# Kernel optimization log

Hardware: AMD Instinct MI355X
Metric: run time of the kernel (lower is better)

The kernel has to match this reference:

```python
import jax, jax.numpy as jnp
import numpy as np

N_NODES = 50000
N_EDGES = 800000
N_GRAPHS = 64
IN_DIM = 128
HID = 32
HEADS = 4
EDGE_DIM = 8
OUT = 10


def setup_inputs() -> dict:
    key = jax.random.key(0)
    ks = jax.random.split(key, 20)
    s = 0.1
    inp = {
        "x": jax.random.normal(ks[0], (N_NODES, IN_DIM), jnp.float32),
        "edge_index": jax.random.randint(ks[1], (2, N_EDGES), 0, N_NODES, jnp.int32),
        "edge_attr": jax.random.normal(ks[2], (N_EDGES, EDGE_DIM), jnp.float32),
        "batch": jnp.sort(jax.random.randint(ks[3], (N_NODES,), 0, N_GRAPHS, jnp.int32)),
        # conv1: heads=4, out=32
        "W1": jax.random.normal(ks[4], (IN_DIM, HEADS * HID), jnp.float32) * s,
        "att_src1": jax.random.normal(ks[5], (HEADS, HID), jnp.float32) * s,
        "att_dst1": jax.random.normal(ks[6], (HEADS, HID), jnp.float32) * s,
        "We1": jax.random.normal(ks[7], (EDGE_DIM, HEADS * HID), jnp.float32) * s,
        "att_e1": jax.random.normal(ks[8], (HEADS, HID), jnp.float32) * s,
        "b1": jnp.zeros((HEADS * HID,), jnp.float32),
        # conv2: heads=1, out=32
        "W2": jax.random.normal(ks[9], (HEADS * HID, HID), jnp.float32) * s,
        "att_src2": jax.random.normal(ks[10], (1, HID), jnp.float32) * s,
        "att_dst2": jax.random.normal(ks[11], (1, HID), jnp.float32) * s,
        "We2": jax.random.normal(ks[12], (EDGE_DIM, HID), jnp.float32) * s,
        "att_e2": jax.random.normal(ks[13], (1, HID), jnp.float32) * s,
        "b2": jnp.zeros((HID,), jnp.float32),
        # MLP head
        "W3": jax.random.normal(ks[14], (HID, HID // 2), jnp.float32) * s,
        "b3": jnp.zeros((HID // 2,), jnp.float32),
        "W4": jax.random.normal(ks[15], (HID // 2, OUT), jnp.float32) * s,
        "b4": jnp.zeros((OUT,), jnp.float32),
    }
    return inp


def _gat_conv(x, src, dst, eattr, W, a_s, a_d, We, a_e, b, H, C, N):
    """PyG GATConv math (self-loops already appended to src/dst/eattr)."""
    h = (x @ W).reshape(-1, H, C)            # [N,H,C]
    e = (eattr @ We).reshape(-1, H, C)       # [E,H,C]
    al_s = jnp.sum(h * a_s, -1)              # [N,H]
    al_d = jnp.sum(h * a_d, -1)              # [N,H]
    alpha = al_s[src] + al_d[dst] + jnp.sum(e * a_e, -1)   # [E,H]
    alpha = jax.nn.leaky_relu(alpha, 0.2)
    # segment softmax over incoming edges of each dst node
    m = jax.ops.segment_max(alpha, dst, num_segments=N)
    ealpha = jnp.exp(alpha - m[dst])
    denom = jax.ops.segment_sum(ealpha, dst, num_segments=N)
    ealpha = ealpha / (denom[dst] + 1e-16)
    msg = h[src] * ealpha[:, :, None]        # [E,H,C]
    out = jax.ops.segment_sum(msg, dst, num_segments=N)  # [N,H,C]
    return out.reshape(N, H * C) + b


def _forward(x, edge_index, edge_attr, batch,
             W1, att_src1, att_dst1, We1, att_e1, b1,
             W2, att_src2, att_dst2, We2, att_e2, b2,
             W3, b3, W4, b4):
    N = x.shape[0]
    src, dst = edge_index[0], edge_index[1]
    # add_self_loops with fill_value='mean': loop attr = mean of incoming edge_attr
    cnt = jax.ops.segment_sum(jnp.ones((src.shape[0],), x.dtype), dst, num_segments=N)
    loop_attr = jax.ops.segment_sum(edge_attr, dst, num_segments=N) / jnp.maximum(cnt, 1.0)[:, None]
    ar = jnp.arange(N, dtype=src.dtype)
    src2 = jnp.concatenate([src, ar])
    dst2 = jnp.concatenate([dst, ar])
    eattr2 = jnp.concatenate([edge_attr, loop_attr], axis=0)

    h = _gat_conv(x, src2, dst2, eattr2, W1, att_src1, att_dst1, We1, att_e1, b1, HEADS, HID, N)
    h = jax.nn.elu(h)
    h = _gat_conv(h, src2, dst2, eattr2, W2, att_src2, att_dst2, We2, att_e2, b2, 1, HID, N)
    h = jax.nn.elu(h)
    # global mean pool per graph
    gsum = jax.ops.segment_sum(h, batch, num_segments=N_GRAPHS)
    gcnt = jax.ops.segment_sum(jnp.ones((N,), h.dtype), batch, num_segments=N_GRAPHS)
    g = gsum / jnp.maximum(gcnt, 1.0)[:, None]
    # MLP head (eval mode: dropout is identity)
    z = jax.nn.relu(g @ W3 + b3)
    return z @ W4 + b4


def reference(x, edge_index, edge_attr, batch,
              W1, att_src1, att_dst1, We1, att_e1, b1,
              W2, att_src2, att_dst2, We2, att_e2, b2,
              W3, b3, W4, b4):
    return _forward(x, edge_index, edge_attr, batch,
                    W1, att_src1, att_dst1, We1, att_e1, b1,
                    W2, att_src2, att_dst2, We2, att_e2, b2,
                    W3, b3, W4, b4)
```

## Files before the change

### kernel.cpp

```cpp
#include <hip/hip_runtime.h>
#include <hip/hip_bf16.h>
#include <math.h>

#define N_NODES 50000
#define N_EDGES 800000
#define N_GRAPHS 64
#define IN_DIM 128
#define HID 32
#define HEADS 4
#define EDGE_DIM 8
#define OUT_DIM 10
#define HC 128
#define NB 196
#define G1H 782

__device__ __forceinline__ float leaky(float x){ return x >= 0.f ? x : 0.2f*x; }
__device__ __forceinline__ float elu_f(float x){ return x > 0.f ? x : __expf(x)-1.f; }

__device__ __forceinline__ float bf2f(unsigned short u){
  union { unsigned int i; float f; } v; v.i = ((unsigned int)u) << 16; return v.f;
}
__device__ __forceinline__ unsigned short f2bf(float f){
  union { float f; unsigned int i; } v; v.f = f;
  unsigned int r = v.i + 0x7FFF + ((v.i >> 16) & 1);
  return (unsigned short)(r >> 16);
}

__device__ __forceinline__ void gemm1_body(int bb, float* xs, float* ws,
    const float* __restrict__ x, const float* __restrict__ W1,
    const float* __restrict__ as1, const float* __restrict__ ad1,
    unsigned short* __restrict__ h1b, float* __restrict__ als1, float* __restrict__ ald1){
  int t = threadIdx.x;
  int cg = t & 15, c8 = cg*8, qb = (t >> 4)*2;
  int base = bb * 32;
  for (int i = t; i < 1024; i += 256){
    int node = base + (i >> 5);
    int col = (i & 31) * 4;
    float4 v = make_float4(0,0,0,0);
    if (node < N_NODES) v = *(const float4*)&x[node*IN_DIM + col];
    *(float4*)&xs[(i>>5)*128 + col] = v;
  }
  float acc[2][8];
  #pragma unroll
  for (int q = 0; q < 2; q++)
    #pragma unroll
    for (int i = 0; i < 8; i++) acc[q][i] = 0.f;

  for (int kb = 0; kb < 128; kb += 32){
    __syncthreads();
    for (int i = t; i < 1024; i += 256)
      *(float4*)&ws[i*4] = *(const float4*)&W1[kb*128 + i*4];
    __syncthreads();
    #pragma unroll 8
    for (int k = 0; k < 32; k++){
      float4 w0 = *(float4*)&ws[k*128 + c8];
      float4 w1 = *(float4*)&ws[k*128 + c8 + 4];
      #pragma unroll
      for (int q = 0; q < 2; q++){
        float xv = xs[(qb + q)*128 + kb + k];
        acc[q][0] = fmaf(xv, w0.x, acc[q][0]);
        acc[q][1] = fmaf(xv, w0.y, acc[q][1]);
        acc[q][2] = fmaf(xv, w0.z, acc[q][2]);
        acc[q][3] = fmaf(xv, w0.w, acc[q][3]);
        acc[q][4] = fmaf(xv, w1.x, acc[q][4]);
        acc[q][5] = fmaf(xv, w1.y, acc[q][5]);
        acc[q][6] = fmaf(xv, w1.z, acc[q][6]);
        acc[q][7] = fmaf(xv, w1.w, acc[q][7]);
      }
    }
  }
  int head = cg >> 2;
  float asv[8], adv[8];
  #pragma unroll
  for (int i = 0; i < 8; i++){ asv[i] = as1[c8 + i]; adv[i] = ad1[c8 + i]; }
  #pragma unroll
  for (int q = 0; q < 2; q++){
    int n = base + qb + q;
    if (n >= N_NODES) continue;
    float sa = 0.f, sd = 0.f;
    #pragma unroll
    for (int i = 0; i < 8; i++){
      sa = fmaf(acc[q][i], asv[i], sa);
      sd = fmaf(acc[q][i], adv[i], sd);
    }
    sa += __shfl_xor(sa, 1); sd += __shfl_xor(sd, 1);
    sa += __shfl_xor(sa, 2); sd += __shfl_xor(sd, 2);
    uint4 pk;
    pk.x = (unsigned int)f2bf(acc[q][0]) | ((unsigned int)f2bf(acc[q][1]) << 16);
    pk.y = (unsigned int)f2bf(acc[q][2]) | ((unsigned int)f2bf(acc[q][3]) << 16);
    pk.z = (unsigned int)f2bf(acc[q][4]) | ((unsigned int)f2bf(acc[q][5]) << 16);
    pk.w = (unsigned int)f2bf(acc[q][6]) | ((unsigned int)f2bf(acc[q][7]) << 16);
    *(uint4*)&h1b[n*HC + c8] = pk;
    if ((cg & 3) == 0){ als1[n*4 + head] = sa; ald1[n*4 + head] = sd; }
  }
}

__global__ __launch_bounds__(256) void k_f1(const int* __restrict__ dst, int* __restrict__ cnt,
    int* __restrict__ rank,
    const float* __restrict__ x, const float* __restrict__ W1,
    const float* __restrict__ as1, const float* __restrict__ ad1,
    unsigned short* __restrict__ h1b, float* __restrict__ als1, float* __restrict__ ald1){
  __shared__ float smem[8192];
  int m = blockIdx.x % 5, r = blockIdx.x / 5;
  if (m < 4){
    int e = (r*4 + m)*256 + threadIdx.x;
    if (e < N_EDGES) rank[e] = atomicAdd(&cnt[dst[e]], 1);
    return;
  }
  gemm1_body(r, smem, smem + 4096, x, W1, as1, ad1, h1b, als1, ald1);
}

__global__ __launch_bounds__(256) void k_blocksum(const int* __restrict__ cnt, int* __restrict__ bsum){
  __shared__ int sh[256];
  int n = blockIdx.x*256 + threadIdx.x;
  sh[threadIdx.x] = (n < N_NODES) ? cnt[n] : 0;
  __syncthreads();
  for (int off = 128; off > 0; off >>= 1){
    if (threadIdx.x < off) sh[threadIdx.x] += sh[threadIdx.x + off];
    __syncthreads();
  }
  if (threadIdx.x == 0) bsum[blockIdx.x] = sh[0];
}

__global__ __launch_bounds__(256) void k_scanb(const int* __restrict__ bsum, int* __restrict__ bpre){
  __shared__ int sh[256];
  int t = threadIdx.x;
  int v = (t < NB) ? bsum[t] : 0;
  sh[t] = v; __syncthreads();
  for (int off = 1; off < 256; off <<= 1){
    int u = (t >= off) ? sh[t-off] : 0;
    __syncthreads();
    sh[t] += u;
    __syncthreads();
  }
  if (t < NB) bpre[t] = sh[t] - v;
}

__global__ __launch_bounds__(256) void k_rowptr(const int* __restrict__ cnt, const int* __restrict__ bpre,
    int* __restrict__ rowptr){
  __shared__ int sh[256];
  int t = threadIdx.x; int n = blockIdx.x*256 + t;
  int c = (n < N_NODES) ? cnt[n] : 0;
  sh[t] = c; __syncthreads();
  for (int off = 1; off < 256; off <<= 1){
    int u = (t >= off) ? sh[t-off] : 0;
    __syncthreads();
    sh[t] += u;
    __syncthreads();
  }
  int incl = sh[t];
  if (n < N_NODES){
    rowptr[n] = bpre[blockIdx.x] + incl - c;
  }
  if (n == N_NODES-1) rowptr[N_NODES] = bpre[blockIdx.x] + incl;
}

__global__ __launch_bounds__(256) void k_f2(const int* __restrict__ src, const int* __restrict__ dst,
    const int* __restrict__ rank, const int* __restrict__ rowptr,
    const float* __restrict__ eattr,
    const float* __restrict__ We1, const float* __restrict__ ae1w,
    const float* __restrict__ We2, const float* __restrict__ ae2w,
    int4* __restrict__ rec,
    const float* __restrict__ x, const float* __restrict__ W1,
    const float* __restrict__ as1, const float* __restrict__ ad1,
    unsigned short* __restrict__ h1b, float* __restrict__ als1, float* __restrict__ ald1){
  __shared__ float smem[8192];
  int m = blockIdx.x % 5, r = blockIdx.x / 5;
  if (m < 4){
    int t = threadIdx.x;
    if (t < 32){
      int d = t >> 2, h = t & 3;
      float s = 0.f;
      for (int c = 0; c < 32; c++) s = fmaf(We1[d*128 + h*32 + c], ae1w[h*32 + c], s);
      smem[d*4 + h] = s;
    } else if (t < 40){
      int d = t - 32;
      float s = 0.f;
      for (int c = 0; c < 32; c++) s = fmaf(We2[d*32 + c], ae2w[c], s);
      smem[32 + d] = s;
    }
    __syncthreads();
    int e = (r*4 + m)*256 + t;
    if (e >= N_EDGES) return;
    int sv = src[e], d = dst[e], rk = rank[e];
    float4 x0 = *(const float4*)&eattr[e*8];
    float4 x1 = *(const float4*)&eattr[e*8+4];
    int pos = rowptr[d] + rk;
    float ea[8] = {x0.x,x0.y,x0.z,x0.w,x1.x,x1.y,x1.z,x1.w};
    float4 rr = make_float4(0,0,0,0);
    float r2 = 0.f;
    #pragma unroll
    for (int dd = 0; dd < 8; dd++){
      rr.x = fmaf(ea[dd], smem[dd*4+0], rr.x);
      rr.y = fmaf(ea[dd], smem[dd*4+1], rr.y);
      rr.z = fmaf(ea[dd], smem[dd*4+2], rr.z);
      rr.w = fmaf(ea[dd], smem[dd*4+3], rr.w);
      r2   = fmaf(ea[dd], smem[32+dd], r2);
    }
    int4 rv;
    rv.x = sv;
    rv.y = (int)((unsigned int)f2bf(rr.x) | ((unsigned int)f2bf(rr.y) << 16));
    rv.z = (int)((unsigned int)f2bf(rr.z) | ((unsigned int)f2bf(rr.w) << 16));
    rv.w = __float_as_int(r2);
    rec[pos] = rv;
    return;
  }
  gemm1_body(G1H + r, smem, smem + 4096, x, W1, as1, ad1, h1b, als1, ald1);
}

__global__ __launch_bounds__(256) void k_conv1(const int* __restrict__ rowptr, const int4* __restrict__ rec,
    const float* __restrict__ als1, const float* __restrict__ ald1,
    const unsigned short* __restrict__ h1b, const float* __restrict__ b1,
    unsigned short* __restrict__ heb){
  int wv = threadIdx.x >> 6, l = threadIdx.x & 63;
  int n = blockIdx.x*4 + wv;
  if (n >= N_NODES) return;
  int c0 = l*2, h = l >> 4;
  int hs1 = (h & 1) * 16;
  float ad = ald1[n*4 + h];
  float den = 0.f, sum_ae = 0.f;
  float2 acc = make_float2(0.f, 0.f);
  int r0 = rowptr[n], r1 = rowptr[n+1];
  int k = r0;
  for (; k + 2 <= r1; k += 2){
    int4 q0 = rec[k], q1 = rec[k+1];
    unsigned int w0 = (h & 2) ? (unsigned int)q0.z : (unsigned int)q0.y;
    unsigned int w1 = (h & 2) ? (unsigned int)q1.z : (unsigned int)q1.y;
    float ae_0 = bf2f((unsigned short)(w0 >> hs1));
    float ae_1 = bf2f((unsigned short)(w1 >> hs1));
    float as_0 = als1[q0.x*4 + h], as_1 = als1[q1.x*4 + h];
    unsigned int hv0 = *(const unsigned int*)(h1b + q0.x*HC + c0);
    unsigned int hv1 = *(const unsigned int*)(h1b + q1.x*HC + c0);
    float p0 = __expf(leaky(as_0 + ad + ae_0));
    float p1 = __expf(leaky(as_1 + ad + ae_1));
    sum_ae += ae_0 + ae_1;
    den += p0 + p1;
    acc.x = fmaf(p0, bf2f((unsigned short)hv0), acc.x);
    acc.y = fmaf(p0, bf2f((unsigned short)(hv0 >> 16)), acc.y);
    acc.x = fmaf(p1, bf2f((unsigned short)hv1), acc.x);
    acc.y = fmaf(p1, bf2f((unsigned short)(hv1 >> 16)), acc.y);
  }
  if (k < r1){
    int4 q = rec[k];
    unsigned int w = (h & 2) ? (unsigned int)q.z : (unsigned int)q.y;
    float aev = bf2f((unsigned short)(w >> hs1));
    float p = __expf(leaky(als1[q.x*4 + h] + ad + aev));
    unsigned int hv = *(const unsigned int*)(h1b + q.x*HC + c0);
    sum_ae += aev; den += p;
    acc.x = fmaf(p, bf2f((unsigned short)hv), acc.x);
    acc.y = fmaf(p, bf2f((unsigned short)(hv >> 16)), acc.y);
  }
  int cn = r1 - r0; if (cn < 1) cn = 1;
  float ps = __expf(leaky(als1[n*4 + h] + ad + sum_ae / (float)cn));
  unsigned int hs = *(const unsigned int*)(h1b + n*HC + c0);
  den += ps;
  acc.x = fmaf(ps, bf2f((unsigned short)hs), acc.x);
  acc.y = fmaf(ps, bf2f((unsigned short)(hs >> 16)), acc.y);
  float inv = 1.f / (den + 1e-16f);
  float o0 = elu_f(fmaf(acc.x, inv, b1[c0]));
  float o1 = elu_f(fmaf(acc.y, inv, b1[c0+1]));
  *(unsigned int*)(heb + n*HC + c0) =
      (unsigned int)f2bf(o0) | ((unsigned int)f2bf(o1) << 16);
}

__global__ __launch_bounds__(256) void k_gemm2(const unsigned short* __restrict__ heb,
    const float* __restrict__ W2, const float* __restrict__ as2, const float* __restrict__ ad2,
    unsigned short* __restrict__ h2b, float* __restrict__ als2, float* __restrict__ ald2){
  __shared__ float ws[128*32];
  __shared__ float xs[16][128];
  int t = threadIdx.x; int c = t & 31; int j = t >> 5;
  int base = blockIdx.x * 16;
  for (int i = t; i < 1024; i += 256)
    *(float4*)&ws[i*4] = *(const float4*)&W2[i*4];
  {
    int node = base + (t >> 4);
    int col = (t & 15) * 8;
    uint4 v = make_uint4(0,0,0,0);
    if (node < N_NODES) v = *(const uint4*)(heb + node*128 + col);
    float* xp = &xs[t>>4][col];
    xp[0] = bf2f((unsigned short)v.x); xp[1] = bf2f((unsigned short)(v.x>>16));
    xp[2] = bf2f((unsigned short)v.y); xp[3] = bf2f((unsigned short)(v.y>>16));
    xp[4] = bf2f((unsigned short)v.z); xp[5] = bf2f((unsigned short)(v.z>>16));
    xp[6] = bf2f((unsigned short)v.w); xp[7] = bf2f((unsigned short)(v.w>>16));
  }
  __syncthreads();
  float s0 = 0.f, s1 = 0.f;
  #pragma unroll 8
  for (int k = 0; k < 128; k++){
    float w = ws[k*32 + c];
    s0 = fmaf(xs[j*2][k],   w, s0);
    s1 = fmaf(xs[j*2+1][k], w, s1);
  }
  float a2c = as2[c], d2c = ad2[c];
  int n0 = base + j*2, n1 = n0 + 1;
  float sa0 = s0*a2c, sd0 = s0*d2c, sa1 = s1*a2c, sd1 = s1*d2c;
  #pragma unroll
  for (int off = 1; off < 32; off <<= 1){
    sa0 += __shfl_xor(sa0, off); sd0 += __shfl_xor(sd0, off);
    sa1 += __shfl_xor(sa1, off); sd1 += __shfl_xor(sd1, off);
  }
  if (n0 < N_NODES){ h2b[n0*32 + c] = f2bf(s0); if (c == 0){ als2[n0] = sa0; ald2[n0] = sd0; } }
  if (n1 < N_NODES){ h2b[n1*32 + c] = f2bf(s1); if (c == 0){ als2[n1] = sa1; ald2[n1] = sd1; } }
}

__global__ __launch_bounds__(256) void k_conv2(const int* __restrict__ rowptr, const int4* __restrict__ rec,
    const float* __restrict__ als2, const float* __restrict__ ald2,
    const unsigned short* __restrict__ h2b, const float* __restrict__ b2, float* __restrict__ out2){
  int wv = threadIdx.x >> 6, l = threadIdx.x & 63;
  int n = blockIdx.x*4 + wv;
  if (n >= N_NODES) return;
  int half = l >> 5, c = l & 31;
  float ad = ald2[n];
  int r0 = rowptr[n], r1 = rowptr[n+1];
  int h0 = (r1 - r0 + 1) >> 1;
  int ks = half ? r0 + h0 : r0;
  int ke = half ? r1 : r0 + h0;
  float den = 0.f, acc = 0.f, sum_ae = 0.f;
  int k = ks;
  for (; k + 2 <= ke; k += 2){
    int4 q0 = rec[k], q1 = rec[k+1];
    float ae_0 = __int_as_float(q0.w), ae_1 = __int_as_float(q1.w);
    float as_0 = als2[q0.x], as_1 = als2[q1.x];
    float hv0 = bf2f(h2b[q0.x*32 + c]);
    float hv1 = bf2f(h2b[q1.x*32 + c]);
    float p0 = __expf(leaky(as_0 + ad + ae_0));
    float p1 = __expf(leaky(as_1 + ad + ae_1));
    sum_ae += ae_0 + ae_1;
    den += p0 + p1;
    acc = fmaf(p0, hv0, acc);
    acc = fmaf(p1, hv1, acc);
  }
  if (k < ke){
    int4 q = rec[k];
    float aev = __int_as_float(q.w);
    float p = __expf(leaky(als2[q.x] + ad + aev));
    float hv = bf2f(h2b[q.x*32 + c]);
    sum_ae += aev; den += p;
    acc = fmaf(p, hv, acc);
  }
  den += __shfl_xor(den, 32);
  acc += __shfl_xor(acc, 32);
  sum_ae += __shfl_xor(sum_ae, 32);
  int cn = r1 - r0; if (cn < 1) cn = 1;
  float ps = __expf(leaky(als2[n] + ad + sum_ae / (float)cn));
  den += ps;
  acc = fmaf(ps, bf2f(h2b[n*32 + c]), acc);
  float val = acc / (den + 1e-16f) + b2[c];
  if (half == 0) out2[n*32 + c] = elu_f(val);
}

__global__ __launch_bounds__(256) void k_pool(const float* __restrict__ out2, const int* __restrict__ batch,
    float* __restrict__ gpool){
  int g = blockIdx.x;
  int a = 0, b = N_NODES;
  while (a < b){ int mid = (a + b) >> 1; if (batch[mid] < g) a = mid + 1; else b = mid; }
  int lo = a;
  a = lo; b = N_NODES;
  while (a < b){ int mid = (a + b) >> 1; if (batch[mid] < g + 1) a = mid + 1; else b = mid; }
  int hi = a;
  int t = threadIdx.x, c = t & 31, r = t >> 5;
  float s = 0.f;
  for (int n = lo + r; n < hi; n += 8) s += out2[n*32 + c];
  __shared__ float sh[256];
  sh[t] = s; __syncthreads();
  if (r == 0){
    for (int q = 1; q < 8; q++) s += sh[q*32 + c];
    int cg = hi - lo; if (cg < 1) cg = 1;
    gpool[g*32 + c] = s / (float)cg;
  }
}

__global__ __launch_bounds__(1024) void k_mlp(const float* __restrict__ gpool, const float* __restrict__ W3,
    const float* __restrict__ b3, const float* __restrict__ W4, const float* __restrict__ b4,
    float* __restrict__ out){
  __shared__ float z[64*16];
  int t = threadIdx.x;
  {
    int g = t >> 4, jj = t & 15;
    float s = b3[jj];
    #pragma unroll
    for (int c = 0; c < 32; c++) s = fmaf(gpool[g*32 + c], W3[c*16 + jj], s);
    z[t] = fmaxf(s, 0.f);
  }
  __syncthreads();
  if (t < 640){
    int g = t / 10, o = t - g*10;
    float s = b4[o];
    #pragma unroll
    for (int jj = 0; jj < 16; jj++) s = fmaf(z[g*16 + jj], W4[jj*10 + o], s);
    out[t] = s;
  }
}

extern "C" void kernel_launch(void* const* d_in, const int* in_sizes, int n_in,
                              void* d_out, int out_size, void* d_ws, size_t ws_size,
                              hipStream_t stream) {
  (void)in_sizes; (void)n_in; (void)out_size; (void)ws_size;
  const float* x     = (const float*)d_in[0];
  const int*   ei    = (const int*)  d_in[1];
  const float* eattr = (const float*)d_in[2];
  const int*   batch = (const int*)  d_in[3];
  const float* W1    = (const float*)d_in[4];
  const float* as1   = (const float*)d_in[5];
  const float* ad1   = (const float*)d_in[6];
  const float* We1   = (const float*)d_in[7];
  const float* ae1w  = (const float*)d_in[8];
  const float* b1    = (const float*)d_in[9];
  const float* W2    = (const float*)d_in[10];
  const float* as2   = (const float*)d_in[11];
  const float* ad2   = (const float*)d_in[12];
  const float* We2   = (const float*)d_in[13];
  const float* ae2w  = (const float*)d_in[14];
  const float* b2    = (const float*)d_in[15];
  const float* W3    = (const float*)d_in[16];
  const float* b3    = (const float*)d_in[17];
  const float* W4    = (const float*)d_in[18];
  const float* b4    = (const float*)d_in[19];
  float* out = (float*)d_out;
  const int* src  = ei;
  const int* dstp = ei + N_EDGES;

  char* p = (char*)d_ws;
  auto alloc = [&](size_t bytes)->void*{ void* r = (void*)p; p += (bytes + 255) & ~(size_t)255; return r; };
  int*    cnt      = (int*)   alloc(4*N_NODES);
  size_t  zero_bytes = (size_t)(p - (char*)d_ws);
  int*    rank     = (int*)   alloc(4*N_EDGES);
  int*    rowptr   = (int*)   alloc(4*(N_NODES+1));
  int*    bsum     = (int*)   alloc(4*NB);
  int*    bpre     = (int*)   alloc(4*NB);
  int4*   rec      = (int4*)  alloc(16*N_EDGES);
  unsigned short* h1b  = (unsigned short*)alloc(2*N_NODES*HC);
  float*  als1     = (float*) alloc(16*N_NODES);
  float*  ald1     = (float*) alloc(16*N_NODES);
  unsigned short* heb  = (unsigned short*)alloc(2*N_NODES*HC);
  unsigned short* h2b  = (unsigned short*)alloc(2*N_NODES*HID);
  float*  als2     = (float*) alloc(4*N_NODES);
  float*  ald2     = (float*) alloc(4*N_NODES);
  float*  out2     = (float*) alloc(4*N_NODES*HID);
  float*  gpool    = (float*) alloc(4*N_GRAPHS*HID);

  const int FGRID = G1H * 5;

  hipMemsetAsync(d_ws, 0, zero_bytes, stream);
  k_f1      <<<FGRID, 256, 0, stream>>>(dstp, cnt, rank, x, W1, as1, ad1, h1b, als1, ald1);
  k_blocksum<<<NB,    256, 0, stream>>>(cnt, bsum);
  k_scanb   <<<1,     256, 0, stream>>>(bsum, bpre);
  k_rowptr  <<<NB,    256, 0, stream>>>(cnt, bpre, rowptr);
  k_f2      <<<FGRID, 256, 0, stream>>>(src, dstp, rank, rowptr, eattr, We1, ae1w, We2, ae2w,
                                        rec, x, W1, as1, ad1, h1b, als1, ald1);
  k_conv1   <<<(N_NODES+3)/4, 256, 0, stream>>>(rowptr, rec, als1, ald1, h1b, b1, heb);
  k_gemm2   <<<(N_NODES+15)/16, 256, 0, stream>>>(heb, W2, as2, ad2, h2b, als2, ald2);
  k_conv2   <<<(N_NODES+3)/4, 256, 0, stream>>>(rowptr, rec, als2, ald2, h2b, b2, out2);
  k_pool    <<<N_GRAPHS, 256, 0, stream>>>(out2, batch, gpool);
  k_mlp     <<<1,    1024, 0, stream>>>(gpool, W3, b3, W4, b4, out);
}
```

Baseline: 371.1 us.

## Split edge loop across lane groups with wide bf16 gathers in conv kernels

Both GAT aggregation kernels now assign each lane a wider slice of feature columns (8 bf16 in conv1, 4 in conv2) and spread the incoming edges of a node across lane groups (4 groups in conv1, 8 in conv2). Partial softmax denominators and accumulators are then combined with xor shuffles. The aim is more independent edge gathers in flight per wavefront and wider vector loads, which cuts the serial edge-loop latency per node. The cost is cross-lane reduction work and more registers per lane.

```diff
diff --git a/kernel.cpp b/kernel.cpp
--- a/kernel.cpp
+++ b/kernel.cpp
@@ -19,6 +19,12 @@
 
 __device__ __forceinline__ float bf2f(unsigned short u){
   union { unsigned int i; float f; } v; v.i = ((unsigned int)u) << 16; return v.f;
+}
+__device__ __forceinline__ float lo16(unsigned int u){
+  union { unsigned int i; float f; } v; v.i = u << 16; return v.f;
+}
+__device__ __forceinline__ float hi16(unsigned int u){
+  union { unsigned int i; float f; } v; v.i = u & 0xffff0000u; return v.f;
 }
 __device__ __forceinline__ unsigned short f2bf(float f){
   union { float f; unsigned int i; } v; v.f = f;
@@ -215,52 +221,70 @@
   int wv = threadIdx.x >> 6, l = threadIdx.x & 63;
   int n = blockIdx.x*4 + wv;
   if (n >= N_NODES) return;
-  int c0 = l*2, h = l >> 4;
+  int g = l >> 4, il = l & 15;
+  int c0 = il*8, h = il >> 2;
   int hs1 = (h & 1) * 16;
   float ad = ald1[n*4 + h];
   float den = 0.f, sum_ae = 0.f;
-  float2 acc = make_float2(0.f, 0.f);
+  float acc[8];
+  #pragma unroll
+  for (int i = 0; i < 8; i++) acc[i] = 0.f;
   int r0 = rowptr[n], r1 = rowptr[n+1];
-  int k = r0;
-  for (; k + 2 <= r1; k += 2){
-    int4 q0 = rec[k], q1 = rec[k+1];
-    unsigned int w0 = (h & 2) ? (unsigned int)q0.z : (unsigned int)q0.y;
-    unsigned int w1 = (h & 2) ? (unsigned int)q1.z : (unsigned int)q1.y;
-    float ae_0 = bf2f((unsigned short)(w0 >> hs1));
-    float ae_1 = bf2f((unsigned short)(w1 >> hs1));
-    float as_0 = als1[q0.x*4 + h], as_1 = als1[q1.x*4 + h];
-    unsigned int hv0 = *(const unsigned int*)(h1b + q0.x*HC + c0);
-    unsigned int hv1 = *(const unsigned int*)(h1b + q1.x*HC + c0);
-    float p0 = __expf(leaky(as_0 + ad + ae_0));
-    float p1 = __expf(leaky(as_1 + ad + ae_1));
-    sum_ae += ae_0 + ae_1;
-    den += p0 + p1;
-    acc.x = fmaf(p0, bf2f((unsigned short)hv0), acc.x);
-    acc.y = fmaf(p0, bf2f((unsigned short)(hv0 >> 16)), acc.y);
-    acc.x = fmaf(p1, bf2f((unsigned short)hv1), acc.x);
-    acc.y = fmaf(p1, bf2f((unsigned short)(hv1 >> 16)), acc.y);
-  }
-  if (k < r1){
+  for (int k = r0 + g; k < r1; k += 4){
     int4 q = rec[k];
     unsigned int w = (h & 2) ? (unsigned int)q.z : (unsigned int)q.y;
     float aev = bf2f((unsigned short)(w >> hs1));
-    float p = __expf(leaky(als1[q.x*4 + h] + ad + aev));
-    unsigned int hv = *(const unsigned int*)(h1b + q.x*HC + c0);
+    float as_v = als1[q.x*4 + h];
+    uint4 hv = *(const uint4*)(h1b + q.x*HC + c0);
+    float p = __expf(leaky(as_v + ad + aev));
     sum_ae += aev; den += p;
-    acc.x = fmaf(p, bf2f((unsigned short)hv), acc.x);
-    acc.y = fmaf(p, bf2f((unsigned short)(hv >> 16)), acc.y);
+    acc[0] = fmaf(p, lo16(hv.x), acc[0]);
+    acc[1] = fmaf(p, hi16(hv.x), acc[1]);
+    acc[2] = fmaf(p, lo16(hv.y), acc[2]);
+    acc[3] = fmaf(p, hi16(hv.y), acc[3]);
+    acc[4] = fmaf(p, lo16(hv.z), acc[4]);
+    acc[5] = fmaf(p, hi16(hv.z), acc[5]);
+    acc[6] = fmaf(p, lo16(hv.w), acc[6]);
+    acc[7] = fmaf(p, hi16(hv.w), acc[7]);
+  }
+  #pragma unroll
+  for (int off = 16; off < 64; off <<= 1){
+    den    += __shfl_xor(den, off);
+    sum_ae += __shfl_xor(sum_ae, off);
+    #pragma unroll
+    for (int i = 0; i < 8; i++) acc[i] += __shfl_xor(acc[i], off);
   }
   int cn = r1 - r0; if (cn < 1) cn = 1;
   float ps = __expf(leaky(als1[n*4 + h] + ad + sum_ae / (float)cn));
-  unsigned int hs = *(const unsigned int*)(h1b + n*HC + c0);
+  uint4 hs = *(const uint4*)(h1b + n*HC + c0);
   den += ps;
-  acc.x = fmaf(ps, bf2f((unsigned short)hs), acc.x);
-  acc.y = fmaf(ps, bf2f((unsigned short)(hs >> 16)), acc.y);
+  acc[0] = fmaf(ps, lo16(hs.x), acc[0]);
+  acc[1] = fmaf(ps, hi16(hs.x), acc[1]);
+  acc[2] = fmaf(ps, lo16(hs.y), acc[2]);
+  acc[3] = fmaf(ps, hi16(hs.y), acc[3]);
+  acc[4] = fmaf(ps, lo16(hs.z), acc[4]);
+  acc[5] = fmaf(ps, hi16(hs.z), acc[5]);
+  acc[6] = fmaf(ps, lo16(hs.w), acc[6]);
+  acc[7] = fmaf(ps, hi16(hs.w), acc[7]);
   float inv = 1.f / (den + 1e-16f);
-  float o0 = elu_f(fmaf(acc.x, inv, b1[c0]));
-  float o1 = elu_f(fmaf(acc.y, inv, b1[c0+1]));
-  *(unsigned int*)(heb + n*HC + c0) =
-      (unsigned int)f2bf(o0) | ((unsigned int)f2bf(o1) << 16);
+  float4 bv0 = *(const float4*)&b1[c0];
+  float4 bv1 = *(const float4*)&b1[c0 + 4];
+  float o0 = elu_f(fmaf(acc[0], inv, bv0.x));
+  float o1 = elu_f(fmaf(acc[1], inv, bv0.y));
+  float o2 = elu_f(fmaf(acc[2], inv, bv0.z));
+  float o3 = elu_f(fmaf(acc[3], inv, bv0.w));
+  float o4 = elu_f(fmaf(acc[4], inv, bv1.x));
+  float o5 = elu_f(fmaf(acc[5], inv, bv1.y));
+  float o6 = elu_f(fmaf(acc[6], inv, bv1.z));
+  float o7 = elu_f(fmaf(acc[7], inv, bv1.w));
+  if (g == 0){
+    uint4 pk;
+    pk.x = (unsigned int)f2bf(o0) | ((unsigned int)f2bf(o1) << 16);
+    pk.y = (unsigned int)f2bf(o2) | ((unsigned int)f2bf(o3) << 16);
+    pk.z = (unsigned int)f2bf(o4) | ((unsigned int)f2bf(o5) << 16);
+    pk.w = (unsigned int)f2bf(o6) | ((unsigned int)f2bf(o7) << 16);
+    *(uint4*)(heb + n*HC + c0) = pk;
+  }
 }
 
 __global__ __launch_bounds__(256) void k_gemm2(const unsigned short* __restrict__ heb,
@@ -309,44 +333,51 @@
   int wv = threadIdx.x >> 6, l = threadIdx.x & 63;
   int n = blockIdx.x*4 + wv;
   if (n >= N_NODES) return;
-  int half = l >> 5, c = l & 31;
+  int g = l >> 3, il = l & 7;
+  int c0 = il*4;
   float ad = ald2[n];
+  float den = 0.f, sum_ae = 0.f;
+  float acc[4];
+  #pragma unroll
+  for (int i = 0; i < 4; i++) acc[i] = 0.f;
   int r0 = rowptr[n], r1 = rowptr[n+1];
-  int h0 = (r1 - r0 + 1) >> 1;
-  int ks = half ? r0 + h0 : r0;
-  int ke = half ? r1 : r0 + h0;
-  float den = 0.f, acc = 0.f, sum_ae = 0.f;
-  int k = ks;
-  for (; k + 2 <= ke; k += 2){
-    int4 q0 = rec[k], q1 = rec[k+1];
-    float ae_0 = __int_as_float(q0.w), ae_1 = __int_as_float(q1.w);
-    float as_0 = als2[q0.x], as_1 = als2[q1.x];
-    float hv0 = bf2f(h2b[q0.x*32 + c]);
-    float hv1 = bf2f(h2b[q1.x*32 + c]);
-    float p0 = __expf(leaky(as_0 + ad + ae_0));
-    float p1 = __expf(leaky(as_1 + ad + ae_1));
-    sum_ae += ae_0 + ae_1;
-    den += p0 + p1;
-    acc = fmaf(p0, hv0, acc);
-    acc = fmaf(p1, hv1, acc);
-  }
-  if (k < ke){
+  for (int k = r0 + g; k < r1; k += 8){
     int4 q = rec[k];
     float aev = __int_as_float(q.w);
-    float p = __expf(leaky(als2[q.x] + ad + aev));
-    float hv = bf2f(h2b[q.x*32 + c]);
+    float as_v = als2[q.x];
+    uint2 hv = *(const uint2*)(h2b + q.x*32 + c0);
+    float p = __expf(leaky(as_v + ad + aev));
     sum_ae += aev; den += p;
-    acc = fmaf(p, hv, acc);
-  }
-  den += __shfl_xor(den, 32);
-  acc += __shfl_xor(acc, 32);
-  sum_ae += __shfl_xor(sum_ae, 32);
+    acc[0] = fmaf(p, lo16(hv.x), acc[0]);
+    acc[1] = fmaf(p, hi16(hv.x), acc[1]);
+    acc[2] = fmaf(p, lo16(hv.y), acc[2]);
+    acc[3] = fmaf(p, hi16(hv.y), acc[3]);
+  }
+  #pragma unroll
+  for (int off = 8; off < 64; off <<= 1){
+    den    += __shfl_xor(den, off);
+    sum_ae += __shfl_xor(sum_ae, off);
+    #pragma unroll
+    for (int i = 0; i < 4; i++) acc[i] += __shfl_xor(acc[i], off);
+  }
   int cn = r1 - r0; if (cn < 1) cn = 1;
   float ps = __expf(leaky(als2[n] + ad + sum_ae / (float)cn));
+  uint2 hs = *(const uint2*)(h2b + n*32 + c0);
   den += ps;
-  acc = fmaf(ps, bf2f(h2b[n*32 + c]), acc);
-  float val = acc / (den + 1e-16f) + b2[c];
-  if (half == 0) out2[n*32 + c] = elu_f(val);
+  acc[0] = fmaf(ps, lo16(hs.x), acc[0]);
+  acc[1] = fmaf(ps, hi16(hs.x), acc[1]);
+  acc[2] = fmaf(ps, lo16(hs.y), acc[2]);
+  acc[3] = fmaf(ps, hi16(hs.y), acc[3]);
+  float inv = 1.f / (den + 1e-16f);
+  float4 bv = *(const float4*)&b2[c0];
+  if (g == 0){
+    float4 ov;
+    ov.x = elu_f(fmaf(acc[0], inv, bv.x));
+    ov.y = elu_f(fmaf(acc[1], inv, bv.y));
+    ov.z = elu_f(fmaf(acc[2], inv, bv.z));
+    ov.w = elu_f(fmaf(acc[3], inv, bv.w));
+    *(float4*)&out2[n*32 + c0] = ov;
+  }
 }
 
 __global__ __launch_bounds__(256) void k_pool(const float* __restrict__ out2, const int* __restrict__ batch,
```

Result: faster. 345.0 us (-7.0%).
